# Optimization experiments

Hardware: AMD Instinct MI355X
Metric: run time of the kernel (lower is better)

Reference implementation:

```python
import jax, jax.numpy as jnp
import numpy as np
import math

N_EMBD = 1024
N_HEAD = 16
B, T = 4, 2048

def setup_inputs() -> dict:
    key = jax.random.key(0)
    k1, k2, k3, k4 = jax.random.split(key, 4)
    x = jax.random.normal(k1, (B, T, N_EMBD), dtype=jnp.float32)
    # torch Linear weights: [out, in]; init scale ~1/sqrt(in)
    s = 1.0 / math.sqrt(N_EMBD)
    W_attn = jax.random.normal(k2, (3 * N_EMBD, N_EMBD), dtype=jnp.float32) * s
    W_proj = jax.random.normal(k3, (N_EMBD, N_EMBD), dtype=jnp.float32) * s
    b_proj = jax.random.normal(k4, (N_EMBD,), dtype=jnp.float32) * s
    return {"x": x, "W_attn": W_attn, "W_proj": W_proj, "b_proj": b_proj}

def reference(x, W_attn, W_proj, b_proj):
    Bx, Tx, C = x.shape
    hd = C // N_HEAD
    qkv = jnp.einsum('btc,oc->bto', x, W_attn)  # [B,T,3C]
    q, k, v = jnp.split(qkv, 3, axis=2)
    # [B, H, T, hd]
    q = q.reshape(Bx, Tx, N_HEAD, hd).transpose(0, 2, 1, 3)
    k = k.reshape(Bx, Tx, N_HEAD, hd).transpose(0, 2, 1, 3)
    v = v.reshape(Bx, Tx, N_HEAD, hd).transpose(0, 2, 1, 3)
    # NOTE: source divides by (1/sqrt(hd)) => MULTIPLIES by sqrt(hd). Faithful.
    att = jnp.einsum('bhqd,bhkd->bhqk', q, k) * jnp.sqrt(jnp.float32(hd))
    causal = jnp.tril(jnp.ones((Tx, Tx), dtype=bool))
    att = jnp.where(causal[None, None, :, :], att, -jnp.inf)
    att = jax.nn.softmax(att, axis=-1)
    y = jnp.einsum('bhqk,bhkd->bhqd', att, v)
    y = y.transpose(0, 2, 1, 3).reshape(Bx, Tx, C)
    y = jnp.einsum('btc,oc->bto', y, W_proj) + b_proj
    return y  # dropout is identity in eval
```

## Files before the change

### kernel.cpp

```cpp
#include <hip/hip_runtime.h>
#include <math.h>

#define BATCH 4
#define TSEQ  2048
#define CEMB  1024
#define NHEAD 16
#define HD    64
#define MROWS (BATCH * TSEQ)
#define QSCALE 11.5415603271f

typedef _Float16 half8 __attribute__((ext_vector_type(8)));
typedef _Float16 half4 __attribute__((ext_vector_type(4)));
typedef float    floatx4 __attribute__((ext_vector_type(4)));

#define GLOBAL_AS __attribute__((address_space(1)))
#define LDS_AS    __attribute__((address_space(3)))

__device__ __forceinline__ void lds_dma16(const _Float16* g, _Float16* l) {
    __builtin_amdgcn_global_load_lds((const GLOBAL_AS unsigned int*)g,
                                     (LDS_AS unsigned int*)l, 16, 0, 0);
}

__device__ __forceinline__ float fast_exp2(float x) {
    float r; asm("v_exp_f32 %0, %1" : "=v"(r) : "v"(x)); return r;
}

__global__ __launch_bounds__(256)
void cvt_fp16(const float* __restrict__ x, const float* __restrict__ wa,
              const float* __restrict__ wp, _Float16* __restrict__ x16,
              _Float16* __restrict__ wa16, _Float16* __restrict__ wp16)
{
    const int n1 = (BATCH * TSEQ * CEMB) / 4;
    const int n2 = (3 * CEMB * CEMB) / 4;
    int i = blockIdx.x * 256 + threadIdx.x;
    const float* src; _Float16* dst; int j;
    if (i < n1)            { src = x;  dst = x16;  j = i; }
    else if (i < n1 + n2)  { src = wa; dst = wa16; j = i - n1; }
    else                   { src = wp; dst = wp16; j = i - n1 - n2; }
    float4 v = ((const float4*)src)[j];
    half4 h = { (_Float16)v.x, (_Float16)v.y, (_Float16)v.z, (_Float16)v.w };
    ((half4*)dst)[j] = h;
}

__device__ __forceinline__ void stage32(const _Float16* __restrict__ gbase,
                                        _Float16* __restrict__ lds,
                                        int row0, int kk, int tid)
{
#pragma unroll
    for (int p = 0; p < 2; ++p) {
        int ci  = p * 256 + tid;
        int row = ci >> 2, pcc = ci & 3;
        int c   = pcc ^ (row & 3);
        lds_dma16(gbase + (size_t)(row0 + row) * CEMB + kk + c * 8, lds + ci * 8);
    }
}

__global__ __launch_bounds__(256)
void qkv_gemm(const _Float16* __restrict__ A, const _Float16* __restrict__ B,
              _Float16* __restrict__ q16, _Float16* __restrict__ k16,
              _Float16* __restrict__ v16)
{
    __shared__ __align__(16) _Float16 smem[16384];
    const int tid = threadIdx.x, lane = tid & 63, wave = tid >> 6;
    const int wm = wave & 1, wn = wave >> 1;
    const int m0 = blockIdx.y * 128, n0 = blockIdx.x * 128;
    const int l15 = lane & 15, quad = lane >> 4;

    floatx4 acc[4][4];
#pragma unroll
    for (int i = 0; i < 4; ++i)
#pragma unroll
        for (int j = 0; j < 4; ++j) acc[i][j] = (floatx4){0.f, 0.f, 0.f, 0.f};

    stage32(A, smem, m0, 0, tid);
    stage32(B, smem + 8192, n0, 0, tid);
    for (int kt = 0; kt < 32; ++kt) {
        const int cur = kt & 1;
        _Float16* Asc = smem + cur * 4096;
        _Float16* Bsc = smem + 8192 + cur * 4096;
        __syncthreads();
        if (kt < 31) {
            stage32(A, smem + (cur ^ 1) * 4096, m0, (kt + 1) * 32, tid);
            stage32(B, smem + 8192 + (cur ^ 1) * 4096, n0, (kt + 1) * 32, tid);
        }
        half8 af[4], bf[4];
#pragma unroll
        for (int mt = 0; mt < 4; ++mt) {
            int row = wm * 64 + mt * 16 + l15;
            af[mt] = *(const half8*)(Asc + row * 32 + (quad ^ (row & 3)) * 8);
        }
#pragma unroll
        for (int nt = 0; nt < 4; ++nt) {
            int row = wn * 64 + nt * 16 + l15;
            bf[nt] = *(const half8*)(Bsc + row * 32 + (quad ^ (row & 3)) * 8);
        }
#pragma unroll
        for (int mt = 0; mt < 4; ++mt)
#pragma unroll
            for (int nt = 0; nt < 4; ++nt)
                acc[mt][nt] = __builtin_amdgcn_mfma_f32_16x16x32_f16(af[mt], bf[nt], acc[mt][nt], 0, 0, 0);
    }

    __syncthreads();
    const int rbase = quad << 2;
    if (n0 < 2 * CEMB) {
        const float scale = (n0 < CEMB) ? QSCALE : 1.0f;
#pragma unroll
        for (int mt = 0; mt < 4; ++mt)
#pragma unroll
            for (int nt = 0; nt < 4; ++nt)
#pragma unroll
                for (int r = 0; r < 4; ++r) {
                    int t = wm * 64 + mt * 16 + rbase + r;
                    int n = wn * 64 + nt * 16 + l15;
                    int pc = (n >> 3) ^ (t & 15);
                    smem[t * 128 + pc * 8 + (n & 7)] = (_Float16)(acc[mt][nt][r] * scale);
                }
        __syncthreads();
        const int chunk = tid & 7;
#pragma unroll
        for (int i = 0; i < 8; ++i) {
            int gr = (tid >> 3) + i * 32;
            int seg = gr >> 7, t = gr & 127;
            int pc = (seg * 8 + chunk) ^ (t & 15);
            half8 v = *(const half8*)(smem + t * 128 + pc * 8);
            int gm = m0 + t, b = gm >> 11, tt = gm & (TSEQ - 1);
            int gnb = n0 + seg * 64;
            _Float16* dst;
            if (n0 < CEMB) {
                int h = gnb >> 6;
                dst = q16 + (((size_t)(b * NHEAD + h)) * TSEQ + tt) * HD;
            } else {
                int h = (gnb - CEMB) >> 6;
                dst = k16 + (((size_t)(b * NHEAD + h)) * TSEQ + tt) * HD;
            }
            *(half8*)(dst + chunk * 8) = v;
        }
    } else {
#pragma unroll
        for (int mt = 0; mt < 4; ++mt)
#pragma unroll
            for (int nt = 0; nt < 4; ++nt)
#pragma unroll
                for (int r = 0; r < 4; ++r) {
                    int t = wm * 64 + mt * 16 + rbase + r;
                    int n = wn * 64 + nt * 16 + l15;
                    int pc = (t >> 3) ^ (n & 15);
                    smem[n * 128 + pc * 8 + (t & 7)] = (_Float16)acc[mt][nt][r];
                }
        __syncthreads();
        const int chunk = tid & 15;
        const int b = m0 >> 11, tblk = m0 & (TSEQ - 1);
#pragma unroll
        for (int i = 0; i < 8; ++i) {
            int row = (tid >> 4) + i * 16;
            int pc = chunk ^ (row & 15);
            half8 v = *(const half8*)(smem + row * 128 + pc * 8);
            int c2 = n0 - 2 * CEMB + row;
            int h = c2 >> 6, d = c2 & 63;
            *(half8*)(v16 + (((size_t)(b * NHEAD + h)) * HD + d) * TSEQ + tblk + chunk * 8) = v;
        }
    }
}

__device__ __forceinline__ void attn_tile(
    const half8& qf0, const half8& qf1,
    float& m_i, float& l_i, floatx4 (&o)[4],
    const _Float16* __restrict__ Ks, const _Float16* __restrict__ Vs,
    bool domask, int l15, int quad, int relq)
{
    floatx4 s[4];
#pragma unroll
    for (int nt = 0; nt < 4; ++nt) {
        int row = nt * 16 + l15;
        int pc0 = quad ^ (row & 7);
        half8 kf0 = *(const half8*)(Ks + row * 64 + pc0 * 8);
        half8 kf1 = *(const half8*)(Ks + row * 64 + (pc0 ^ 4) * 8);
        floatx4 z = (floatx4){0.f, 0.f, 0.f, 0.f};
        z = __builtin_amdgcn_mfma_f32_16x16x32_f16(kf0, qf0, z, 0, 0, 0);
        z = __builtin_amdgcn_mfma_f32_16x16x32_f16(kf1, qf1, z, 0, 0, 0);
        s[nt] = z;
    }
    if (domask) {
#pragma unroll
        for (int nt = 0; nt < 4; ++nt)
#pragma unroll
            for (int r = 0; r < 4; ++r)
                if (nt * 16 + quad * 4 + r > relq) s[nt][r] = -INFINITY;
    }
    float mx = m_i;
#pragma unroll
    for (int nt = 0; nt < 4; ++nt)
        mx = fmaxf(mx, fmaxf(fmaxf(s[nt][0], s[nt][1]), fmaxf(s[nt][2], s[nt][3])));
    mx = fmaxf(mx, __shfl_xor(mx, 16, 64));
    mx = fmaxf(mx, __shfl_xor(mx, 32, 64));
    float alpha = fast_exp2(m_i - mx);
    m_i = mx;
    float rs = 0.f;
    half4 p[4];
#pragma unroll
    for (int nt = 0; nt < 4; ++nt) {
        float p0 = fast_exp2(s[nt][0] - mx), p1 = fast_exp2(s[nt][1] - mx);
        float p2 = fast_exp2(s[nt][2] - mx), p3 = fast_exp2(s[nt][3] - mx);
        rs += (p0 + p1) + (p2 + p3);
        p[nt] = (half4){ (_Float16)p0, (_Float16)p1, (_Float16)p2, (_Float16)p3 };
    }
    rs += __shfl_xor(rs, 16, 64);
    rs += __shfl_xor(rs, 32, 64);
    l_i = l_i * alpha + rs;
#pragma unroll
    for (int mt = 0; mt < 4; ++mt)
#pragma unroll
        for (int r = 0; r < 4; ++r) o[mt][r] *= alpha;
#pragma unroll
    for (int mt = 0; mt < 4; ++mt) {
        int d = mt * 16 + l15;
#pragma unroll
        for (int nt = 0; nt < 4; ++nt) {
            int pc = (2 * nt + (quad >> 1)) ^ (d & 7);
            half4 vf = *(const half4*)(Vs + d * 64 + pc * 8 + (quad & 1) * 4);
            o[mt] = __builtin_amdgcn_mfma_f32_16x16x16f16(vf, p[nt], o[mt], 0, 0, 0);
        }
    }
}

__device__ __forceinline__ void attn_tile2(
    const half8& qA0, const half8& qA1, const half8& qB0, const half8& qB1,
    float& mAi, float& lAi, floatx4 (&oA)[4],
    float& mBi, float& lBi, floatx4 (&oB)[4],
    const _Float16* __restrict__ Ks, const _Float16* __restrict__ Vs,
    bool maskA, int l15, int quad, int relq)
{
    floatx4 sA[4], sB[4];
#pragma unroll
    for (int nt = 0; nt < 4; ++nt) {
        int row = nt * 16 + l15;
        int pc0 = quad ^ (row & 7);
        half8 kf0 = *(const half8*)(Ks + row * 64 + pc0 * 8);
        half8 kf1 = *(const half8*)(Ks + row * 64 + (pc0 ^ 4) * 8);
        floatx4 zA = (floatx4){0.f, 0.f, 0.f, 0.f};
        floatx4 zB = (floatx4){0.f, 0.f, 0.f, 0.f};
        zA = __builtin_amdgcn_mfma_f32_16x16x32_f16(kf0, qA0, zA, 0, 0, 0);
        zB = __builtin_amdgcn_mfma_f32_16x16x32_f16(kf0, qB0, zB, 0, 0, 0);
        zA = __builtin_amdgcn_mfma_f32_16x16x32_f16(kf1, qA1, zA, 0, 0, 0);
        zB = __builtin_amdgcn_mfma_f32_16x16x32_f16(kf1, qB1, zB, 0, 0, 0);
        sA[nt] = zA; sB[nt] = zB;
    }
    if (maskA) {
#pragma unroll
        for (int nt = 0; nt < 4; ++nt)
#pragma unroll
            for (int r = 0; r < 4; ++r)
                if (nt * 16 + quad * 4 + r > relq) sA[nt][r] = -INFINITY;
    }
    float mxA = mAi, mxB = mBi;
#pragma unroll
    for (int nt = 0; nt < 4; ++nt) {
        mxA = fmaxf(mxA, fmaxf(fmaxf(sA[nt][0], sA[nt][1]), fmaxf(sA[nt][2], sA[nt][3])));
        mxB = fmaxf(mxB, fmaxf(fmaxf(sB[nt][0], sB[nt][1]), fmaxf(sB[nt][2], sB[nt][3])));
    }
    mxA = fmaxf(mxA, __shfl_xor(mxA, 16, 64));
    mxB = fmaxf(mxB, __shfl_xor(mxB, 16, 64));
    mxA = fmaxf(mxA, __shfl_xor(mxA, 32, 64));
    mxB = fmaxf(mxB, __shfl_xor(mxB, 32, 64));
    float alA = fast_exp2(mAi - mxA);
    float alB = fast_exp2(mBi - mxB);
    mAi = mxA; mBi = mxB;
    float rsA = 0.f, rsB = 0.f;
    half4 pA[4], pB[4];
#pragma unroll
    for (int nt = 0; nt < 4; ++nt) {
        float a0 = fast_exp2(sA[nt][0] - mxA), b0 = fast_exp2(sB[nt][0] - mxB);
        float a1 = fast_exp2(sA[nt][1] - mxA), b1 = fast_exp2(sB[nt][1] - mxB);
        float a2 = fast_exp2(sA[nt][2] - mxA), b2 = fast_exp2(sB[nt][2] - mxB);
        float a3 = fast_exp2(sA[nt][3] - mxA), b3 = fast_exp2(sB[nt][3] - mxB);
        rsA += (a0 + a1) + (a2 + a3);
        rsB += (b0 + b1) + (b2 + b3);
        pA[nt] = (half4){ (_Float16)a0, (_Float16)a1, (_Float16)a2, (_Float16)a3 };
        pB[nt] = (half4){ (_Float16)b0, (_Float16)b1, (_Float16)b2, (_Float16)b3 };
    }
    rsA += __shfl_xor(rsA, 16, 64);
    rsB += __shfl_xor(rsB, 16, 64);
    rsA += __shfl_xor(rsA, 32, 64);
    rsB += __shfl_xor(rsB, 32, 64);
    lAi = lAi * alA + rsA;
    lBi = lBi * alB + rsB;
#pragma unroll
    for (int mt = 0; mt < 4; ++mt)
#pragma unroll
        for (int r = 0; r < 4; ++r) { oA[mt][r] *= alA; oB[mt][r] *= alB; }
#pragma unroll
    for (int mt = 0; mt < 4; ++mt) {
        int d = mt * 16 + l15;
#pragma unroll
        for (int nt = 0; nt < 4; ++nt) {
            int pc = (2 * nt + (quad >> 1)) ^ (d & 7);
            half4 vf = *(const half4*)(Vs + d * 64 + pc * 8 + (quad & 1) * 4);
            oA[mt] = __builtin_amdgcn_mfma_f32_16x16x16f16(vf, pA[nt], oA[mt], 0, 0, 0);
            oB[mt] = __builtin_amdgcn_mfma_f32_16x16x16f16(vf, pB[nt], oB[mt], 0, 0, 0);
        }
    }
}

__global__ __launch_bounds__(256)
void attn_fwd(const _Float16* __restrict__ q16, const _Float16* __restrict__ k16,
              const _Float16* __restrict__ v16, _Float16* __restrict__ o16)
{
    __shared__ __align__(16) _Float16 Ks[2][64 * 64];
    __shared__ __align__(16) _Float16 Vs[2][64 * 64];
    const int tid = threadIdx.x, lane = tid & 63, wave = tid >> 6;
    const int l15 = lane & 15, quad = lane >> 4;
    const int qtA = blockIdx.x;
    const int qtB = 31 - qtA;
    const int bh = blockIdx.y, b = bh >> 4, h = bh & 15;
    const int q0A = qtA * 64, q0B = qtB * 64;
    const _Float16* qp = q16 + (size_t)bh * TSEQ * HD;
    const _Float16* kp = k16 + (size_t)bh * TSEQ * HD;
    const _Float16* vp = v16 + (size_t)bh * HD * TSEQ;

    const int relq = wave * 16 + l15;
    half8 qA0 = *(const half8*)(qp + (size_t)(q0A + relq) * HD + quad * 8);
    half8 qA1 = *(const half8*)(qp + (size_t)(q0A + relq) * HD + 32 + quad * 8);
    half8 qB0 = *(const half8*)(qp + (size_t)(q0B + relq) * HD + quad * 8);
    half8 qB1 = *(const half8*)(qp + (size_t)(q0B + relq) * HD + 32 + quad * 8);

    float mA = -INFINITY, lA = 0.f, mB = -INFINITY, lB = 0.f;
    floatx4 oA[4], oB[4];
#pragma unroll
    for (int mt = 0; mt < 4; ++mt) { oA[mt] = (floatx4){0.f,0.f,0.f,0.f}; oB[mt] = (floatx4){0.f,0.f,0.f,0.f}; }

#define STAGE_KV(kt0, buf)                                                     \
    {                                                                          \
        _Float16* kd = Ks[buf];                                                \
        _Float16* vd = Vs[buf];                                                \
        _Pragma("unroll")                                                      \
        for (int p = 0; p < 2; ++p) {                                          \
            int ci = p * 256 + tid;                                            \
            int row = ci >> 3;                                                 \
            int c = (ci & 7) ^ (row & 7);                                      \
            lds_dma16(kp + (size_t)((kt0) + row) * HD + c * 8, kd + ci * 8);   \
            lds_dma16(vp + (size_t)row * TSEQ + (kt0) + c * 8, vd + ci * 8);   \
        }                                                                      \
    }

    STAGE_KV(0, 0);
    for (int kt = 0; kt <= qtA; ++kt) {
        const int cur = kt & 1;
        __syncthreads();
        STAGE_KV((kt + 1) * 64, cur ^ 1);
        attn_tile2(qA0, qA1, qB0, qB1, mA, lA, oA, mB, lB, oB,
                   Ks[cur], Vs[cur], (kt == qtA), l15, quad, relq);
    }
    for (int kt = qtA + 1; kt <= qtB; ++kt) {
        const int cur = kt & 1;
        __syncthreads();
        if (kt < qtB) STAGE_KV((kt + 1) * 64, cur ^ 1);
        attn_tile(qB0, qB1, mB, lB, oB, Ks[cur], Vs[cur], (kt == qtB), l15, quad, relq);
    }
#undef STAGE_KV

    const float invA = 1.f / lA, invB = 1.f / lB;
    const size_t baseA = ((size_t)(b * TSEQ + q0A + relq)) * CEMB + h * HD + quad * 4;
    const size_t baseB = ((size_t)(b * TSEQ + q0B + relq)) * CEMB + h * HD + quad * 4;
#pragma unroll
    for (int mt = 0; mt < 4; ++mt) {
        half4 ha = { (_Float16)(oA[mt][0] * invA), (_Float16)(oA[mt][1] * invA),
                     (_Float16)(oA[mt][2] * invA), (_Float16)(oA[mt][3] * invA) };
        half4 hb = { (_Float16)(oB[mt][0] * invB), (_Float16)(oB[mt][1] * invB),
                     (_Float16)(oB[mt][2] * invB), (_Float16)(oB[mt][3] * invB) };
        *(half4*)(o16 + baseA + mt * 16) = ha;
        *(half4*)(o16 + baseB + mt * 16) = hb;
    }
}

__global__ __launch_bounds__(256)
void proj_gemm(const _Float16* __restrict__ A, const _Float16* __restrict__ B,
               const float* __restrict__ bias, float* __restrict__ out)
{
    __shared__ __align__(16) _Float16 As2[2][64 * 32];
    __shared__ __align__(16) _Float16 Bs2[2][128 * 32];
    const int tid = threadIdx.x, lane = tid & 63, wave = tid >> 6;
    const int wm = wave & 1, wn = wave >> 1;
    const int m0 = blockIdx.y * 64, n0 = blockIdx.x * 128;
    const int l15 = lane & 15, quad = lane >> 4;

    floatx4 acc[2][4];
#pragma unroll
    for (int i = 0; i < 2; ++i)
#pragma unroll
        for (int j = 0; j < 4; ++j) acc[i][j] = (floatx4){0.f, 0.f, 0.f, 0.f};

#define STAGE_A(kk, buf)                                                       \
    {                                                                          \
        int row = tid >> 2, c = (tid & 3) ^ (row & 3);                         \
        lds_dma16(A + (size_t)(m0 + row) * CEMB + (kk) + c * 8,                \
                  As2[buf] + tid * 8);                                         \
    }

    STAGE_A(0, 0);
    stage32(B, Bs2[0], n0, 0, tid);
    for (int kt = 0; kt < 32; ++kt) {
        const int cur = kt & 1;
        __syncthreads();
        if (kt < 31) {
            STAGE_A((kt + 1) * 32, cur ^ 1);
            stage32(B, Bs2[cur ^ 1], n0, (kt + 1) * 32, tid);
        }
        half8 af[2], bf[4];
#pragma unroll
        for (int mt = 0; mt < 2; ++mt) {
            int row = wm * 32 + mt * 16 + l15;
            af[mt] = *(const half8*)(As2[cur] + row * 32 + (quad ^ (row & 3)) * 8);
        }
#pragma unroll
        for (int nt = 0; nt < 4; ++nt) {
            int row = wn * 64 + nt * 16 + l15;
            bf[nt] = *(const half8*)(Bs2[cur] + row * 32 + (quad ^ (row & 3)) * 8);
        }
#pragma unroll
        for (int mt = 0; mt < 2; ++mt)
#pragma unroll
            for (int nt = 0; nt < 4; ++nt)
                acc[mt][nt] = __builtin_amdgcn_mfma_f32_16x16x32_f16(af[mt], bf[nt], acc[mt][nt], 0, 0, 0);
    }
#undef STAGE_A

    const int rbase = quad << 2;
#pragma unroll
    for (int mt = 0; mt < 2; ++mt)
#pragma unroll
        for (int nt = 0; nt < 4; ++nt) {
            int gn = n0 + wn * 64 + nt * 16 + l15;
            float bb = bias[gn];
#pragma unroll
            for (int r = 0; r < 4; ++r) {
                int gm = m0 + wm * 32 + mt * 16 + rbase + r;
                out[(size_t)gm * CEMB + gn] = acc[mt][nt][r] + bb;
            }
        }
}

extern "C" void kernel_launch(void* const* d_in, const int* in_sizes, int n_in,
                              void* d_out, int out_size, void* d_ws, size_t ws_size,
                              hipStream_t stream) {
    const float* x     = (const float*)d_in[0];
    const float* Wattn = (const float*)d_in[1];
    const float* Wproj = (const float*)d_in[2];
    const float* bproj = (const float*)d_in[3];
    float* out = (float*)d_out;

    const size_t nx  = (size_t)BATCH * TSEQ * CEMB;
    const size_t nwa = (size_t)3 * CEMB * CEMB;
    const size_t nwp = (size_t)CEMB * CEMB;
    const size_t per = (size_t)BATCH * NHEAD * TSEQ * HD;

    _Float16* x16    = (_Float16*)d_ws;
    _Float16* wa16   = x16 + nx;
    _Float16* wp16   = wa16 + nwa;
    _Float16* q16    = wp16 + nwp;
    _Float16* k16    = q16 + per;
    _Float16* v16    = k16 + per;
    _Float16* attn16 = x16;

    const int nconv = (int)((nx + nwa + nwp) / 4);
    cvt_fp16<<<nconv / 256, 256, 0, stream>>>(x, Wattn, Wproj, x16, wa16, wp16);
    qkv_gemm<<<dim3(3 * CEMB / 128, MROWS / 128), 256, 0, stream>>>(x16, wa16, q16, k16, v16);
    attn_fwd<<<dim3(16, BATCH * NHEAD), 256, 0, stream>>>(q16, k16, v16, attn16);
    proj_gemm<<<dim3(CEMB / 128, MROWS / 64), 256, 0, stream>>>(attn16, wp16, bproj, out);
}
```

Before: 299.1 us.

## Rebalance attention waves across paired query tiles and skip redundant rescaling

Work inside each attention block is redistributed so that two waves handle query tile A and two handle tile B, each wave covering 32 rows, in place of every wave covering 16 rows of both tiles. The A-tile waves sit idle for the later key tiles. The online-softmax rescale and the cross-lane max reduction are skipped when no lane's maximum grows, and the row-sum reduction is deferred until the end. The block index is also remapped to group heads for cache locality. The aim is fewer per-tile shuffles and exponentials, traded against wave imbalance and a divergent branch.

```diff
diff --git a/kernel.cpp b/kernel.cpp
--- a/kernel.cpp
+++ b/kernel.cpp
@@ -163,73 +163,12 @@
     }
 }
 
-__device__ __forceinline__ void attn_tile(
-    const half8& qf0, const half8& qf1,
-    float& m_i, float& l_i, floatx4 (&o)[4],
-    const _Float16* __restrict__ Ks, const _Float16* __restrict__ Vs,
-    bool domask, int l15, int quad, int relq)
-{
-    floatx4 s[4];
-#pragma unroll
-    for (int nt = 0; nt < 4; ++nt) {
-        int row = nt * 16 + l15;
-        int pc0 = quad ^ (row & 7);
-        half8 kf0 = *(const half8*)(Ks + row * 64 + pc0 * 8);
-        half8 kf1 = *(const half8*)(Ks + row * 64 + (pc0 ^ 4) * 8);
-        floatx4 z = (floatx4){0.f, 0.f, 0.f, 0.f};
-        z = __builtin_amdgcn_mfma_f32_16x16x32_f16(kf0, qf0, z, 0, 0, 0);
-        z = __builtin_amdgcn_mfma_f32_16x16x32_f16(kf1, qf1, z, 0, 0, 0);
-        s[nt] = z;
-    }
-    if (domask) {
-#pragma unroll
-        for (int nt = 0; nt < 4; ++nt)
-#pragma unroll
-            for (int r = 0; r < 4; ++r)
-                if (nt * 16 + quad * 4 + r > relq) s[nt][r] = -INFINITY;
-    }
-    float mx = m_i;
-#pragma unroll
-    for (int nt = 0; nt < 4; ++nt)
-        mx = fmaxf(mx, fmaxf(fmaxf(s[nt][0], s[nt][1]), fmaxf(s[nt][2], s[nt][3])));
-    mx = fmaxf(mx, __shfl_xor(mx, 16, 64));
-    mx = fmaxf(mx, __shfl_xor(mx, 32, 64));
-    float alpha = fast_exp2(m_i - mx);
-    m_i = mx;
-    float rs = 0.f;
-    half4 p[4];
-#pragma unroll
-    for (int nt = 0; nt < 4; ++nt) {
-        float p0 = fast_exp2(s[nt][0] - mx), p1 = fast_exp2(s[nt][1] - mx);
-        float p2 = fast_exp2(s[nt][2] - mx), p3 = fast_exp2(s[nt][3] - mx);
-        rs += (p0 + p1) + (p2 + p3);
-        p[nt] = (half4){ (_Float16)p0, (_Float16)p1, (_Float16)p2, (_Float16)p3 };
-    }
-    rs += __shfl_xor(rs, 16, 64);
-    rs += __shfl_xor(rs, 32, 64);
-    l_i = l_i * alpha + rs;
-#pragma unroll
-    for (int mt = 0; mt < 4; ++mt)
-#pragma unroll
-        for (int r = 0; r < 4; ++r) o[mt][r] *= alpha;
-#pragma unroll
-    for (int mt = 0; mt < 4; ++mt) {
-        int d = mt * 16 + l15;
-#pragma unroll
-        for (int nt = 0; nt < 4; ++nt) {
-            int pc = (2 * nt + (quad >> 1)) ^ (d & 7);
-            half4 vf = *(const half4*)(Vs + d * 64 + pc * 8 + (quad & 1) * 4);
-            o[mt] = __builtin_amdgcn_mfma_f32_16x16x16f16(vf, p[nt], o[mt], 0, 0, 0);
-        }
-    }
-}
-
-__device__ __forceinline__ void attn_tile2(
+__device__ __forceinline__ void attn_tile_pair(
     const half8& qA0, const half8& qA1, const half8& qB0, const half8& qB1,
     float& mAi, float& lAi, floatx4 (&oA)[4],
     float& mBi, float& lBi, floatx4 (&oB)[4],
     const _Float16* __restrict__ Ks, const _Float16* __restrict__ Vs,
-    bool maskA, int l15, int quad, int relq)
+    bool diag, int l15, int quad, int relqA)
 {
     floatx4 sA[4], sB[4];
 #pragma unroll
@@ -246,49 +185,52 @@
         zB = __builtin_amdgcn_mfma_f32_16x16x32_f16(kf1, qB1, zB, 0, 0, 0);
         sA[nt] = zA; sB[nt] = zB;
     }
-    if (maskA) {
+    if (diag) {
+        const int relqB = relqA + 16;
 #pragma unroll
         for (int nt = 0; nt < 4; ++nt)
 #pragma unroll
-            for (int r = 0; r < 4; ++r)
-                if (nt * 16 + quad * 4 + r > relq) sA[nt][r] = -INFINITY;
-    }
-    float mxA = mAi, mxB = mBi;
+            for (int r = 0; r < 4; ++r) {
+                int rk = nt * 16 + quad * 4 + r;
+                if (rk > relqA) sA[nt][r] = -INFINITY;
+                if (rk > relqB) sB[nt][r] = -INFINITY;
+            }
+    }
+    float pA = -INFINITY, pB = -INFINITY;
 #pragma unroll
     for (int nt = 0; nt < 4; ++nt) {
-        mxA = fmaxf(mxA, fmaxf(fmaxf(sA[nt][0], sA[nt][1]), fmaxf(sA[nt][2], sA[nt][3])));
-        mxB = fmaxf(mxB, fmaxf(fmaxf(sB[nt][0], sB[nt][1]), fmaxf(sB[nt][2], sB[nt][3])));
-    }
-    mxA = fmaxf(mxA, __shfl_xor(mxA, 16, 64));
-    mxB = fmaxf(mxB, __shfl_xor(mxB, 16, 64));
-    mxA = fmaxf(mxA, __shfl_xor(mxA, 32, 64));
-    mxB = fmaxf(mxB, __shfl_xor(mxB, 32, 64));
-    float alA = fast_exp2(mAi - mxA);
-    float alB = fast_exp2(mBi - mxB);
-    mAi = mxA; mBi = mxB;
+        pA = fmaxf(pA, fmaxf(fmaxf(sA[nt][0], sA[nt][1]), fmaxf(sA[nt][2], sA[nt][3])));
+        pB = fmaxf(pB, fmaxf(fmaxf(sB[nt][0], sB[nt][1]), fmaxf(sB[nt][2], sB[nt][3])));
+    }
+    if (!__all((pA <= mAi) && (pB <= mBi))) {
+        float mxA = fmaxf(mAi, pA), mxB = fmaxf(mBi, pB);
+        mxA = fmaxf(mxA, __shfl_xor(mxA, 16, 64));
+        mxB = fmaxf(mxB, __shfl_xor(mxB, 16, 64));
+        mxA = fmaxf(mxA, __shfl_xor(mxA, 32, 64));
+        mxB = fmaxf(mxB, __shfl_xor(mxB, 32, 64));
+        float alA = fast_exp2(mAi - mxA);
+        float alB = fast_exp2(mBi - mxB);
+        mAi = mxA; mBi = mxB;
+        lAi *= alA; lBi *= alB;
+#pragma unroll
+        for (int mt = 0; mt < 4; ++mt)
+#pragma unroll
+            for (int r = 0; r < 4; ++r) { oA[mt][r] *= alA; oB[mt][r] *= alB; }
+    }
     float rsA = 0.f, rsB = 0.f;
-    half4 pA[4], pB[4];
+    half4 pAh[4], pBh[4];
 #pragma unroll
     for (int nt = 0; nt < 4; ++nt) {
-        float a0 = fast_exp2(sA[nt][0] - mxA), b0 = fast_exp2(sB[nt][0] - mxB);
-        float a1 = fast_exp2(sA[nt][1] - mxA), b1 = fast_exp2(sB[nt][1] - mxB);
-        float a2 = fast_exp2(sA[nt][2] - mxA), b2 = fast_exp2(sB[nt][2] - mxB);
-        float a3 = fast_exp2(sA[nt][3] - mxA), b3 = fast_exp2(sB[nt][3] - mxB);
+        float a0 = fast_exp2(sA[nt][0] - mAi), b0 = fast_exp2(sB[nt][0] - mBi);
+        float a1 = fast_exp2(sA[nt][1] - mAi), b1 = fast_exp2(sB[nt][1] - mBi);
+        float a2 = fast_exp2(sA[nt][2] - mAi), b2 = fast_exp2(sB[nt][2] - mBi);
+        float a3 = fast_exp2(sA[nt][3] - mAi), b3 = fast_exp2(sB[nt][3] - mBi);
         rsA += (a0 + a1) + (a2 + a3);
         rsB += (b0 + b1) + (b2 + b3);
-        pA[nt] = (half4){ (_Float16)a0, (_Float16)a1, (_Float16)a2, (_Float16)a3 };
-        pB[nt] = (half4){ (_Float16)b0, (_Float16)b1, (_Float16)b2, (_Float16)b3 };
-    }
-    rsA += __shfl_xor(rsA, 16, 64);
-    rsB += __shfl_xor(rsB, 16, 64);
-    rsA += __shfl_xor(rsA, 32, 64);
-    rsB += __shfl_xor(rsB, 32, 64);
-    lAi = lAi * alA + rsA;
-    lBi = lBi * alB + rsB;
-#pragma unroll
-    for (int mt = 0; mt < 4; ++mt)
-#pragma unroll
-        for (int r = 0; r < 4; ++r) { oA[mt][r] *= alA; oB[mt][r] *= alB; }
+        pAh[nt] = (half4){ (_Float16)a0, (_Float16)a1, (_Float16)a2, (_Float16)a3 };
+        pBh[nt] = (half4){ (_Float16)b0, (_Float16)b1, (_Float16)b2, (_Float16)b3 };
+    }
+    lAi += rsA; lBi += rsB;
 #pragma unroll
     for (int mt = 0; mt < 4; ++mt) {
         int d = mt * 16 + l15;
@@ -296,8 +238,8 @@
         for (int nt = 0; nt < 4; ++nt) {
             int pc = (2 * nt + (quad >> 1)) ^ (d & 7);
             half4 vf = *(const half4*)(Vs + d * 64 + pc * 8 + (quad & 1) * 4);
-            oA[mt] = __builtin_amdgcn_mfma_f32_16x16x16f16(vf, pA[nt], oA[mt], 0, 0, 0);
-            oB[mt] = __builtin_amdgcn_mfma_f32_16x16x16f16(vf, pB[nt], oB[mt], 0, 0, 0);
+            oA[mt] = __builtin_amdgcn_mfma_f32_16x16x16f16(vf, pAh[nt], oA[mt], 0, 0, 0);
+            oB[mt] = __builtin_amdgcn_mfma_f32_16x16x16f16(vf, pBh[nt], oB[mt], 0, 0, 0);
         }
     }
 }
@@ -308,21 +250,27 @@
 {
     __shared__ __align__(16) _Float16 Ks[2][64 * 64];
     __shared__ __align__(16) _Float16 Vs[2][64 * 64];
-    const int tid = threadIdx.x, lane = tid & 63, wave = tid >> 6;
+    const int tid = threadIdx.x, lane = tid & 63, wv = tid >> 6;
     const int l15 = lane & 15, quad = lane >> 4;
-    const int qtA = blockIdx.x;
+
+    const int L   = blockIdx.x + 16 * blockIdx.y;
+    const int qtA = (L >> 3) & 15;
+    const int bh  = (L & 7) + ((L >> 7) << 3);
     const int qtB = 31 - qtA;
-    const int bh = blockIdx.y, b = bh >> 4, h = bh & 15;
-    const int q0A = qtA * 64, q0B = qtB * 64;
+    const int b = bh >> 4, h = bh & 15;
+
     const _Float16* qp = q16 + (size_t)bh * TSEQ * HD;
     const _Float16* kp = k16 + (size_t)bh * TSEQ * HD;
     const _Float16* vp = v16 + (size_t)bh * HD * TSEQ;
 
-    const int relq = wave * 16 + l15;
-    half8 qA0 = *(const half8*)(qp + (size_t)(q0A + relq) * HD + quad * 8);
-    half8 qA1 = *(const half8*)(qp + (size_t)(q0A + relq) * HD + 32 + quad * 8);
-    half8 qB0 = *(const half8*)(qp + (size_t)(q0B + relq) * HD + quad * 8);
-    half8 qB1 = *(const half8*)(qp + (size_t)(q0B + relq) * HD + 32 + quad * 8);
+    const int myqt  = (wv < 2) ? qtA : qtB;
+    const int relqA = (wv & 1) * 32 + l15;
+    const int rowA  = myqt * 64 + relqA;
+
+    half8 qA0 = *(const half8*)(qp + (size_t)rowA * HD + quad * 8);
+    half8 qA1 = *(const half8*)(qp + (size_t)rowA * HD + 32 + quad * 8);
+    half8 qB0 = *(const half8*)(qp + (size_t)(rowA + 16) * HD + quad * 8);
+    half8 qB1 = *(const half8*)(qp + (size_t)(rowA + 16) * HD + 32 + quad * 8);
 
     float mA = -INFINITY, lA = 0.f, mB = -INFINITY, lB = 0.f;
     floatx4 oA[4], oB[4];
@@ -344,24 +292,21 @@
     }
 
     STAGE_KV(0, 0);
-    for (int kt = 0; kt <= qtA; ++kt) {
-        const int cur = kt & 1;
-        __syncthreads();
-        STAGE_KV((kt + 1) * 64, cur ^ 1);
-        attn_tile2(qA0, qA1, qB0, qB1, mA, lA, oA, mB, lB, oB,
-                   Ks[cur], Vs[cur], (kt == qtA), l15, quad, relq);
-    }
-    for (int kt = qtA + 1; kt <= qtB; ++kt) {
+    for (int kt = 0; kt <= qtB; ++kt) {
         const int cur = kt & 1;
         __syncthreads();
         if (kt < qtB) STAGE_KV((kt + 1) * 64, cur ^ 1);
-        attn_tile(qB0, qB1, mB, lB, oB, Ks[cur], Vs[cur], (kt == qtB), l15, quad, relq);
+        if (kt <= myqt)
+            attn_tile_pair(qA0, qA1, qB0, qB1, mA, lA, oA, mB, lB, oB,
+                           Ks[cur], Vs[cur], kt == myqt, l15, quad, relqA);
     }
 #undef STAGE_KV
 
+    lA += __shfl_xor(lA, 16, 64); lA += __shfl_xor(lA, 32, 64);
+    lB += __shfl_xor(lB, 16, 64); lB += __shfl_xor(lB, 32, 64);
     const float invA = 1.f / lA, invB = 1.f / lB;
-    const size_t baseA = ((size_t)(b * TSEQ + q0A + relq)) * CEMB + h * HD + quad * 4;
-    const size_t baseB = ((size_t)(b * TSEQ + q0B + relq)) * CEMB + h * HD + quad * 4;
+    const size_t baseA = ((size_t)(b * TSEQ + rowA)) * CEMB + h * HD + quad * 4;
+    const size_t baseB = baseA + (size_t)16 * CEMB;
 #pragma unroll
     for (int mt = 0; mt < 4; ++mt) {
         half4 ha = { (_Float16)(oA[mt][0] * invA), (_Float16)(oA[mt][1] * invA),
```

Result: no change. 304.7 us (+1.9%).

## Skip online-softmax rescale when max unchanged, defer row-sum reduction, remap block order

Applied to the files above, without the earlier changes.

The attention inner loop now computes the tile max per lane and performs the cross-lane max reduction and accumulator rescale only when some lane's max actually grows, a wave-uniform branch. The row-sum shuffle reduction is moved out of the loop and done once before normalisation, since lane-partial sums stay consistent under uniform rescaling. Block indices are also remapped so that consecutive workgroups cover eight heads at the same query tile, which changes L2 locality. This trades a vote and a branch for fewer shuffles and multiplies per tile.

```diff
diff --git a/kernel.cpp b/kernel.cpp
--- a/kernel.cpp
+++ b/kernel.cpp
@@ -188,30 +188,32 @@
             for (int r = 0; r < 4; ++r)
                 if (nt * 16 + quad * 4 + r > relq) s[nt][r] = -INFINITY;
     }
-    float mx = m_i;
+    float pmax = -INFINITY;
 #pragma unroll
     for (int nt = 0; nt < 4; ++nt)
-        mx = fmaxf(mx, fmaxf(fmaxf(s[nt][0], s[nt][1]), fmaxf(s[nt][2], s[nt][3])));
-    mx = fmaxf(mx, __shfl_xor(mx, 16, 64));
-    mx = fmaxf(mx, __shfl_xor(mx, 32, 64));
-    float alpha = fast_exp2(m_i - mx);
-    m_i = mx;
+        pmax = fmaxf(pmax, fmaxf(fmaxf(s[nt][0], s[nt][1]), fmaxf(s[nt][2], s[nt][3])));
+    if (!__all(pmax <= m_i)) {
+        float mx = fmaxf(m_i, pmax);
+        mx = fmaxf(mx, __shfl_xor(mx, 16, 64));
+        mx = fmaxf(mx, __shfl_xor(mx, 32, 64));
+        float alpha = fast_exp2(m_i - mx);
+        m_i = mx;
+        l_i *= alpha;
+#pragma unroll
+        for (int mt = 0; mt < 4; ++mt)
+#pragma unroll
+            for (int r = 0; r < 4; ++r) o[mt][r] *= alpha;
+    }
     float rs = 0.f;
     half4 p[4];
 #pragma unroll
     for (int nt = 0; nt < 4; ++nt) {
-        float p0 = fast_exp2(s[nt][0] - mx), p1 = fast_exp2(s[nt][1] - mx);
-        float p2 = fast_exp2(s[nt][2] - mx), p3 = fast_exp2(s[nt][3] - mx);
+        float p0 = fast_exp2(s[nt][0] - m_i), p1 = fast_exp2(s[nt][1] - m_i);
+        float p2 = fast_exp2(s[nt][2] - m_i), p3 = fast_exp2(s[nt][3] - m_i);
         rs += (p0 + p1) + (p2 + p3);
         p[nt] = (half4){ (_Float16)p0, (_Float16)p1, (_Float16)p2, (_Float16)p3 };
     }
-    rs += __shfl_xor(rs, 16, 64);
-    rs += __shfl_xor(rs, 32, 64);
-    l_i = l_i * alpha + rs;
-#pragma unroll
-    for (int mt = 0; mt < 4; ++mt)
-#pragma unroll
-        for (int r = 0; r < 4; ++r) o[mt][r] *= alpha;
+    l_i += rs;
 #pragma unroll
     for (int mt = 0; mt < 4; ++mt) {
         int d = mt * 16 + l15;
@@ -253,42 +255,41 @@
             for (int r = 0; r < 4; ++r)
                 if (nt * 16 + quad * 4 + r > relq) sA[nt][r] = -INFINITY;
     }
-    float mxA = mAi, mxB = mBi;
+    float pA = -INFINITY, pB = -INFINITY;
 #pragma unroll
     for (int nt = 0; nt < 4; ++nt) {
-        mxA = fmaxf(mxA, fmaxf(fmaxf(sA[nt][0], sA[nt][1]), fmaxf(sA[nt][2], sA[nt][3])));
-        mxB = fmaxf(mxB, fmaxf(fmaxf(sB[nt][0], sB[nt][1]), fmaxf(sB[nt][2], sB[nt][3])));
-    }
-    mxA = fmaxf(mxA, __shfl_xor(mxA, 16, 64));
-    mxB = fmaxf(mxB, __shfl_xor(mxB, 16, 64));
-    mxA = fmaxf(mxA, __shfl_xor(mxA, 32, 64));
-    mxB = fmaxf(mxB, __shfl_xor(mxB, 32, 64));
-    float alA = fast_exp2(mAi - mxA);
-    float alB = fast_exp2(mBi - mxB);
-    mAi = mxA; mBi = mxB;
+        pA = fmaxf(pA, fmaxf(fmaxf(sA[nt][0], sA[nt][1]), fmaxf(sA[nt][2], sA[nt][3])));
+        pB = fmaxf(pB, fmaxf(fmaxf(sB[nt][0], sB[nt][1]), fmaxf(sB[nt][2], sB[nt][3])));
+    }
+    if (!__all((pA <= mAi) && (pB <= mBi))) {
+        float mxA = fmaxf(mAi, pA), mxB = fmaxf(mBi, pB);
+        mxA = fmaxf(mxA, __shfl_xor(mxA, 16, 64));
+        mxB = fmaxf(mxB, __shfl_xor(mxB, 16, 64));
+        mxA = fmaxf(mxA, __shfl_xor(mxA, 32, 64));
+        mxB = fmaxf(mxB, __shfl_xor(mxB, 32, 64));
+        float alA = fast_exp2(mAi - mxA);
+        float alB = fast_exp2(mBi - mxB);
+        mAi = mxA; mBi = mxB;
+        lAi *= alA; lBi *= alB;
+#pragma unroll
+        for (int mt = 0; mt < 4; ++mt)
+#pragma unroll
+            for (int r = 0; r < 4; ++r) { oA[mt][r] *= alA; oB[mt][r] *= alB; }
+    }
     float rsA = 0.f, rsB = 0.f;
-    half4 pA[4], pB[4];
+    half4 pAh[4], pBh[4];
 #pragma unroll
     for (int nt = 0; nt < 4; ++nt) {
-        float a0 = fast_exp2(sA[nt][0] - mxA), b0 = fast_exp2(sB[nt][0] - mxB);
-        float a1 = fast_exp2(sA[nt][1] - mxA), b1 = fast_exp2(sB[nt][1] - mxB);
-        float a2 = fast_exp2(sA[nt][2] - mxA), b2 = fast_exp2(sB[nt][2] - mxB);
-        float a3 = fast_exp2(sA[nt][3] - mxA), b3 = fast_exp2(sB[nt][3] - mxB);
+        float a0 = fast_exp2(sA[nt][0] - mAi), b0 = fast_exp2(sB[nt][0] - mBi);
+        float a1 = fast_exp2(sA[nt][1] - mAi), b1 = fast_exp2(sB[nt][1] - mBi);
+        float a2 = fast_exp2(sA[nt][2] - mAi), b2 = fast_exp2(sB[nt][2] - mBi);
+        float a3 = fast_exp2(sA[nt][3] - mAi), b3 = fast_exp2(sB[nt][3] - mBi);
         rsA += (a0 + a1) + (a2 + a3);
         rsB += (b0 + b1) + (b2 + b3);
-        pA[nt] = (half4){ (_Float16)a0, (_Float16)a1, (_Float16)a2, (_Float16)a3 };
-        pB[nt] = (half4){ (_Float16)b0, (_Float16)b1, (_Float16)b2, (_Float16)b3 };
-    }
-    rsA += __shfl_xor(rsA, 16, 64);
-    rsB += __shfl_xor(rsB, 16, 64);
-    rsA += __shfl_xor(rsA, 32, 64);
-    rsB += __shfl_xor(rsB, 32, 64);
-    lAi = lAi * alA + rsA;
-    lBi = lBi * alB + rsB;
-#pragma unroll
-    for (int mt = 0; mt < 4; ++mt)
-#pragma unroll
-        for (int r = 0; r < 4; ++r) { oA[mt][r] *= alA; oB[mt][r] *= alB; }
+        pAh[nt] = (half4){ (_Float16)a0, (_Float16)a1, (_Float16)a2, (_Float16)a3 };
+        pBh[nt] = (half4){ (_Float16)b0, (_Float16)b1, (_Float16)b2, (_Float16)b3 };
+    }
+    lAi += rsA; lBi += rsB;
 #pragma unroll
     for (int mt = 0; mt < 4; ++mt) {
         int d = mt * 16 + l15;
@@ -296,8 +297,8 @@
         for (int nt = 0; nt < 4; ++nt) {
             int pc = (2 * nt + (quad >> 1)) ^ (d & 7);
             half4 vf = *(const half4*)(Vs + d * 64 + pc * 8 + (quad & 1) * 4);
-            oA[mt] = __builtin_amdgcn_mfma_f32_16x16x16f16(vf, pA[nt], oA[mt], 0, 0, 0);
-            oB[mt] = __builtin_amdgcn_mfma_f32_16x16x16f16(vf, pB[nt], oB[mt], 0, 0, 0);
+            oA[mt] = __builtin_amdgcn_mfma_f32_16x16x16f16(vf, pAh[nt], oA[mt], 0, 0, 0);
+            oB[mt] = __builtin_amdgcn_mfma_f32_16x16x16f16(vf, pBh[nt], oB[mt], 0, 0, 0);
         }
     }
 }
@@ -310,9 +311,12 @@
     __shared__ __align__(16) _Float16 Vs[2][64 * 64];
     const int tid = threadIdx.x, lane = tid & 63, wave = tid >> 6;
     const int l15 = lane & 15, quad = lane >> 4;
-    const int qtA = blockIdx.x;
+
+    const int L   = blockIdx.x + 16 * blockIdx.y;
+    const int qtA = (L >> 3) & 15;
+    const int bh  = (L & 7) + ((L >> 7) << 3);
     const int qtB = 31 - qtA;
-    const int bh = blockIdx.y, b = bh >> 4, h = bh & 15;
+    const int b = bh >> 4, h = bh & 15;
     const int q0A = qtA * 64, q0B = qtB * 64;
     const _Float16* qp = q16 + (size_t)bh * TSEQ * HD;
     const _Float16* kp = k16 + (size_t)bh * TSEQ * HD;
@@ -359,6 +363,8 @@
     }
 #undef STAGE_KV
 
+    lA += __shfl_xor(lA, 16, 64); lA += __shfl_xor(lA, 32, 64);
+    lB += __shfl_xor(lB, 16, 64); lB += __shfl_xor(lB, 32, 64);
     const float invA = 1.f / lA, invB = 1.f / lB;
     const size_t baseA = ((size_t)(b * TSEQ + q0A + relq)) * CEMB + h * HD + quad * 4;
     const size_t baseB = ((size_t)(b * TSEQ + q0B + relq)) * CEMB + h * HD + quad * 4;
```

After: 283.7 us. 1.05x faster.
